# Optimization experiments

Hardware: AMD Instinct MI355X
Metric: run time of the kernel (lower is better)

Reference implementation:

```python
import jax, jax.numpy as jnp
import numpy as np

DIM = 768
NUM_HEADS = 12
HEAD_DIM = DIM // NUM_HEADS
SCALE = HEAD_DIM ** -0.5


def setup_inputs() -> dict:
    key = jax.random.key(0)
    k1, k2, k3, k4 = jax.random.split(key, 4)
    B, H, W = 8, 32, 32
    x = jax.random.normal(k1, (B, H, W, DIM), dtype=jnp.float32)
    s = DIM ** -0.5
    w_qkv = jax.random.normal(k2, (DIM, 3 * DIM), dtype=jnp.float32) * s
    w_proj = jax.random.normal(k3, (DIM, DIM), dtype=jnp.float32) * s
    b_proj = jax.random.normal(k4, (DIM,), dtype=jnp.float32) * 0.01
    return {"x": x, "w_qkv": w_qkv, "w_proj": w_proj, "b_proj": b_proj}


def reference(x, w_qkv, w_proj, b_proj):
    B, H, W, C = x.shape
    N = H * W
    qkv = (x.reshape(B, N, C) @ w_qkv).reshape(B, N, 3, NUM_HEADS, HEAD_DIM)
    q, k, v = jnp.moveaxis(qkv, 2, 0)  # each (B, N, h, d)
    # scores: (B, h, N, N)
    attn = jnp.einsum('bnhd,bmhd->bhnm', q * SCALE, k)
    attn = jax.nn.softmax(attn, axis=-1)
    out = jnp.einsum('bhnm,bmhd->bnhd', attn, v).reshape(B, H, W, C)
    return out @ w_proj + b_proj
```

## Files before the change

kernel.cpp:

```cpp
#include <hip/hip_runtime.h>

typedef _Float16 half_t;
typedef __attribute__((ext_vector_type(4))) _Float16 half4;
typedef __attribute__((ext_vector_type(8))) _Float16 half8;
typedef __attribute__((ext_vector_type(4))) float floatx4;

#define MFMA_F16(A,B,C)  __builtin_amdgcn_mfma_f32_16x16x32_f16(A,B,C,0,0,0)

typedef __attribute__((address_space(1))) const void gvoid_t;
typedef __attribute__((address_space(3))) void svoid_t;

__device__ __forceinline__ void async_copy16(const half_t* g, half_t* l) {
    __builtin_amdgcn_global_load_lds((gvoid_t*)g, (svoid_t*)l, 16, 0, 0);
}

#define QSCALE 0.18033688011112042f

__global__ __launch_bounds__(256)
void prep_kernel(const float* __restrict__ x, const float* __restrict__ w_qkv,
                 const float* __restrict__ w_proj, half_t* __restrict__ xh,
                 half_t* __restrict__ wqkvT, half_t* __restrict__ wprojT)
{
    __shared__ half_t tile[64 * 65];
    const int id = blockIdx.x, tid = threadIdx.x;
    if (id < 6144) {
        size_t e = (size_t)id * 1024 + tid * 4;
        float4 f = *(const float4*)(x + e);
        half4 h = { (half_t)f.x, (half_t)f.y, (half_t)f.z, (half_t)f.w };
        *(half4*)(xh + e) = h;
        return;
    }
    const float* src; half_t* dst; int lds, tr0, tc0;
    if (id < 6576) { int t = id - 6144; src = w_qkv; dst = wqkvT; lds = 2304;
                     tr0 = (t / 36) * 64; tc0 = (t % 36) * 64; }
    else           { int t = id - 6576; src = w_proj; dst = wprojT; lds = 768;
                     tr0 = (t / 12) * 64; tc0 = (t % 12) * 64; }
    #pragma unroll
    for (int i = 0; i < 4; i++) {
        int e = tid + i * 256, r = e >> 4, c4 = (e & 15) << 2;
        float4 f = *(const float4*)(src + (size_t)(tr0 + r) * lds + tc0 + c4);
        tile[(c4 + 0) * 65 + r] = (half_t)f.x;
        tile[(c4 + 1) * 65 + r] = (half_t)f.y;
        tile[(c4 + 2) * 65 + r] = (half_t)f.z;
        tile[(c4 + 3) * 65 + r] = (half_t)f.w;
    }
    __syncthreads();
    #pragma unroll
    for (int i = 0; i < 4; i++) {
        int e = tid + i * 256, c = e >> 4, r4 = (e & 15) << 2;
        half4 h = { tile[c * 65 + r4], tile[c * 65 + r4 + 1],
                    tile[c * 65 + r4 + 2], tile[c * 65 + r4 + 3] };
        *(half4*)(dst + (size_t)(tc0 + c) * 768 + tr0 + r4) = h;
    }
}

__global__ __launch_bounds__(512, 1)
void gemm_qkv(const half_t* __restrict__ A, const half_t* __restrict__ Bt,
              half_t* __restrict__ q_ws, half_t* __restrict__ k_ws,
              half_t* __restrict__ v_ws)
{
    __shared__ half_t As[2][256 * 32];
    __shared__ half_t Bs[2][288 * 32];

    const int lin  = blockIdx.x;
    const int xcd  = lin & 7, rest = lin >> 3;
    const int m0 = ((rest >> 3) * 8 + xcd) * 256;
    const int n0 = (rest & 7) * 288;

    const int tid  = threadIdx.x;
    const int lane = tid & 63;
    const int w    = tid >> 6;
    const int wm   = w >> 1, wn = w & 1;
    const int quad = lane >> 4, l16 = lane & 15;

    const int b0p = (lane ^ (lane >> 2) ^ (lane >> 4)) & 1;
    const int b1p = ((lane >> 1) ^ (lane >> 3)) & 1;
    const int b2p = ((lane >> 2) ^ (lane >> 4)) & 1;
    const int row_log = ((lane >> 2) & 0xC) | ((lane >> 2) & 2) | b2p;
    const int q_log   = (b1p << 1) | b0p;

    const int foff = ((((l16 << 2) | quad) ^ (l16 & 7)) << 3);

    const half_t* aBase = A  + (size_t)(m0 + row_log) * 768 + q_log * 8;
    const half_t* bBase = Bt + (size_t)(n0 + row_log) * 768 + q_log * 8;

    floatx4 acc[4][9];
    #pragma unroll
    for (int i = 0; i < 4; i++)
        #pragma unroll
        for (int j = 0; j < 9; j++) acc[i][j] = (floatx4)0.0f;

    half8 sA0, sA1, sB0, sB1, sB2;

    #define LOADR(KO)                                                          \
        do {                                                                   \
            sA0 = *(const half8*)(aBase + (size_t)((w*2+0)*16) * 768 + (KO));  \
            sA1 = *(const half8*)(aBase + (size_t)((w*2+1)*16) * 768 + (KO));  \
            sB0 = *(const half8*)(bBase + (size_t)((w*2+0)*16) * 768 + (KO));  \
            sB1 = *(const half8*)(bBase + (size_t)((w*2+1)*16) * 768 + (KO));  \
            if (w < 2)                                                         \
                sB2 = *(const half8*)(bBase + (size_t)((16+w)*16) * 768 + (KO)); \
        } while (0)

    #define WRITES(BUF)                                                        \
        do {                                                                   \
            *(half8*)(&As[BUF][(w*2+0)*512 + lane*8]) = sA0;                   \
            *(half8*)(&As[BUF][(w*2+1)*512 + lane*8]) = sA1;                   \
            *(half8*)(&Bs[BUF][(w*2+0)*512 + lane*8]) = sB0;                   \
            *(half8*)(&Bs[BUF][(w*2+1)*512 + lane*8]) = sB1;                   \
            if (w < 2)                                                         \
                *(half8*)(&Bs[BUF][(16+w)*512 + lane*8]) = sB2;                \
        } while (0)

    LOADR(0);
    WRITES(0);
    __syncthreads();

    #pragma unroll 1
    for (int t = 0; t < 24; ++t) {
        const int cur = t & 1;
        if (t < 23) LOADR((t + 1) * 32);

        half8 a[4], b[9];
        #pragma unroll
        for (int mi = 0; mi < 4; mi++)
            a[mi] = *(const half8*)(&As[cur][(wm*4 + mi) * 512 + foff]);
        #pragma unroll
        for (int ni = 0; ni < 9; ni++)
            b[ni] = *(const half8*)(&Bs[cur][(wn*9 + ni) * 512 + foff]);
        __builtin_amdgcn_s_setprio(1);
        #pragma unroll
        for (int mi = 0; mi < 4; mi++)
            #pragma unroll
            for (int ni = 0; ni < 9; ni++)
                acc[mi][ni] = MFMA_F16(a[mi], b[ni], acc[mi][ni]);
        __builtin_amdgcn_s_setprio(0);

        if (t < 23) WRITES(cur ^ 1);
        __syncthreads();
    }
    #undef LOADR
    #undef WRITES

    const int bb  = (m0 + wm * 64) >> 10;
    const int t0w = (m0 + wm * 64) & 1023;

    #pragma unroll
    for (int ni = 0; ni < 9; ni++) {
        const int cb  = n0 + wn * 144 + ni * 16;
        const int sel = (cb >= 1536) ? 2 : (cb >= 768 ? 1 : 0);
        const int rem = cb - sel * 768;
        const int hh  = rem >> 6;
        const int d   = (rem & 63) + l16;
        const size_t base = (size_t)(bb * 12 + hh) * 65536;

        if (sel == 0) {
            #pragma unroll
            for (int mi = 0; mi < 4; mi++) {
                int tok = t0w + mi * 16 + quad * 4;
                half4 hv = { (half_t)(acc[mi][ni][0] * QSCALE),
                             (half_t)(acc[mi][ni][1] * QSCALE),
                             (half_t)(acc[mi][ni][2] * QSCALE),
                             (half_t)(acc[mi][ni][3] * QSCALE) };
                *(half4*)(q_ws + base + (size_t)d * 1024 + tok) = hv;
            }
        } else if (sel == 1) {
            #pragma unroll
            for (int mi = 0; mi < 4; mi++)
                #pragma unroll
                for (int r = 0; r < 4; r++) {
                    int tok = t0w + mi * 16 + quad * 4 + r;
                    k_ws[base + (size_t)tok * 64 + d] = (half_t)acc[mi][ni][r];
                }
        } else {
            #pragma unroll
            for (int mi = 0; mi < 4; mi++) {
                int tokb = t0w + (mi >> 1) * 32;
                int tokp = tokb | (quad << 3) | ((mi & 1) << 2);
                half4 hv = { (half_t)acc[mi][ni][0], (half_t)acc[mi][ni][1],
                             (half_t)acc[mi][ni][2], (half_t)acc[mi][ni][3] };
                *(half4*)(v_ws + base + (size_t)d * 1024 + tokp) = hv;
            }
        }
    }
}

__global__ __launch_bounds__(256, 2)
void gemm_proj(const half_t* __restrict__ A, const half_t* __restrict__ Bt,
               float* __restrict__ Cout, const float* __restrict__ bias)
{
    __shared__ half_t As[2][128 * 32];
    __shared__ half_t Bs[2][192 * 32];

    const int lin  = blockIdx.x;
    const int xcd  = lin & 7, rest = lin >> 3;
    const int m0 = ((rest >> 2) * 8 + xcd) * 128;
    const int n0 = (rest & 3) * 192;

    const int tid  = threadIdx.x;
    const int lane = tid & 63;
    const int w    = tid >> 6;
    const int wm   = w >> 1, wn = w & 1;
    const int quad = lane >> 4, l16 = lane & 15;

    const int b0p = (lane ^ (lane >> 2) ^ (lane >> 4)) & 1;
    const int b1p = ((lane >> 1) ^ (lane >> 3)) & 1;
    const int b2p = ((lane >> 2) ^ (lane >> 4)) & 1;
    const int row_log = ((lane >> 2) & 0xC) | ((lane >> 2) & 2) | b2p;
    const int q_log   = (b1p << 1) | b0p;
    const int foff = ((((l16 << 2) | quad) ^ (l16 & 7)) << 3);

    const half_t* aBase = A  + (size_t)(m0 + row_log) * 768 + q_log * 8;
    const half_t* bBase = Bt + (size_t)(n0 + row_log) * 768 + q_log * 8;

    floatx4 acc[4][6];
    #pragma unroll
    for (int i = 0; i < 4; i++)
        #pragma unroll
        for (int j = 0; j < 6; j++) acc[i][j] = (floatx4)0.0f;

    half8 sA0, sA1, sB0, sB1, sB2;

    #define PLOADR(KO)                                                         \
        do {                                                                   \
            sA0 = *(const half8*)(aBase + (size_t)((w*2+0)*16) * 768 + (KO));  \
            sA1 = *(const half8*)(aBase + (size_t)((w*2+1)*16) * 768 + (KO));  \
            sB0 = *(const half8*)(bBase + (size_t)((w*3+0)*16) * 768 + (KO));  \
            sB1 = *(const half8*)(bBase + (size_t)((w*3+1)*16) * 768 + (KO));  \
            sB2 = *(const half8*)(bBase + (size_t)((w*3+2)*16) * 768 + (KO));  \
        } while (0)

    #define PWRITES(BUF)                                                       \
        do {                                                                   \
            *(half8*)(&As[BUF][(w*2+0)*512 + lane*8]) = sA0;                   \
            *(half8*)(&As[BUF][(w*2+1)*512 + lane*8]) = sA1;                   \
            *(half8*)(&Bs[BUF][(w*3+0)*512 + lane*8]) = sB0;                   \
            *(half8*)(&Bs[BUF][(w*3+1)*512 + lane*8]) = sB1;                   \
            *(half8*)(&Bs[BUF][(w*3+2)*512 + lane*8]) = sB2;                   \
        } while (0)

    PLOADR(0);
    PWRITES(0);
    __syncthreads();

    #pragma unroll 1
    for (int t = 0; t < 24; ++t) {
        const int cur = t & 1;
        if (t < 23) PLOADR((t + 1) * 32);

        half8 a[4], b[6];
        #pragma unroll
        for (int mi = 0; mi < 4; mi++)
            a[mi] = *(const half8*)(&As[cur][(wm*4 + mi) * 512 + foff]);
        #pragma unroll
        for (int ni = 0; ni < 6; ni++)
            b[ni] = *(const half8*)(&Bs[cur][(wn*6 + ni) * 512 + foff]);
        __builtin_amdgcn_s_setprio(1);
        #pragma unroll
        for (int mi = 0; mi < 4; mi++)
            #pragma unroll
            for (int ni = 0; ni < 6; ni++)
                acc[mi][ni] = MFMA_F16(a[mi], b[ni], acc[mi][ni]);
        __builtin_amdgcn_s_setprio(0);

        if (t < 23) PWRITES(cur ^ 1);
        __syncthreads();
    }
    #undef PLOADR
    #undef PWRITES

    float bias_v[6];
    #pragma unroll
    for (int ni = 0; ni < 6; ni++)
        bias_v[ni] = bias[n0 + wn * 96 + ni * 16 + l16];
    float* scratch = (w < 2 ? (float*)As : (float*)Bs) + (w & 1) * 1600;
    #pragma unroll
    for (int mi = 0; mi < 4; mi++) {
        #pragma unroll
        for (int ni = 0; ni < 6; ni++)
            #pragma unroll
            for (int r = 0; r < 4; r++)
                scratch[(quad * 4 + r) * 100 + ni * 16 + l16] =
                    acc[mi][ni][r] + bias_v[ni];
        #pragma unroll
        for (int i = 0; i < 6; i++) {
            int f = quad + i * 4;
            float4 v4 = *(const float4*)(scratch + l16 * 100 + f * 4);
            int gm = m0 + wm * 64 + mi * 16 + l16;
            *(float4*)(Cout + (size_t)gm * 768 + n0 + wn * 96 + f * 4) = v4;
        }
    }
}

__global__ __launch_bounds__(256, 3)
void attn_kernel(const half_t* __restrict__ qT, const half_t* __restrict__ k,
                 const half_t* __restrict__ vT, half_t* __restrict__ a_ws)
{
    __shared__ __align__(16) half_t Kb[2][4096];
    __shared__ __align__(16) half_t Vb[2][4096];
    __shared__ __align__(16) half_t Qs[64 * 128];

    const int lin  = blockIdx.x;
    const int xcd  = lin & 7, rest = lin >> 3;
    const int qc   = rest & 7;
    const int bh   = (rest >> 3) * 8 + xcd;

    const int tid  = threadIdx.x;
    const int lane = tid & 63;
    const int w    = tid >> 6;
    const int quad = lane >> 4, l16 = lane & 15;

    const half_t* qg = qT + (size_t)bh * 65536;
    const half_t* kg = k  + (size_t)bh * 65536;
    const half_t* vg = vT + (size_t)bh * 65536;

    const int srow = lane >> 3;
    const int sch  = (lane & 7) ^ srow;

    #pragma unroll
    for (int j = 0; j < 4; j++) {
        int d0 = w * 16 + j * 4;
        async_copy16(qg + (size_t)(d0 + (lane >> 4)) * 1024 + qc * 128 + (lane & 15) * 8,
                     &Qs[d0 * 128]);
    }
    #pragma unroll
    for (int j = 0; j < 2; j++) {
        int row = j * 32 + w * 8;
        async_copy16(kg + (size_t)(row + srow) * 64 + sch * 8, &Kb[0][row * 64]);
        async_copy16(vg + (size_t)(row + srow) * 1024 + sch * 8, &Vb[0][row * 64]);
    }
    __syncthreads();

    half8 qf[2][2];
    #pragma unroll
    for (int T = 0; T < 2; T++)
        #pragma unroll
        for (int ks = 0; ks < 2; ks++)
            #pragma unroll
            for (int j = 0; j < 8; j++)
                qf[T][ks][j] = Qs[(ks * 32 + quad * 8 + j) * 128
                                  + T * 64 + w * 16 + l16];

    floatx4 acc_o[2][4];
    floatx4 lacc[2];
    #pragma unroll
    for (int T = 0; T < 2; T++) {
        lacc[T] = (floatx4)0.0f;
        #pragma unroll
        for (int dt = 0; dt < 4; dt++) acc_o[T][dt] = (floatx4)0.0f;
    }

    const int xsw = l16 & 7;
    const half8 vone = { (half_t)1.0f, (half_t)1.0f, (half_t)1.0f, (half_t)1.0f,
                         (half_t)1.0f, (half_t)1.0f, (half_t)1.0f, (half_t)1.0f };

    half8 rk0, rk1, rv0, rv1;

    for (int kt = 0; kt < 16; kt++) {
        const int cb = kt & 1;
        __syncthreads();
        if (kt < 15) {
            rk0 = *(const half8*)(kg + (size_t)((kt + 1) * 64 + w * 8 + srow) * 64 + sch * 8);
            rk1 = *(const half8*)(kg + (size_t)((kt + 1) * 64 + 32 + w * 8 + srow) * 64 + sch * 8);
            rv0 = *(const half8*)(vg + (size_t)(w * 8 + srow) * 1024 + (kt + 1) * 64 + sch * 8);
            rv1 = *(const half8*)(vg + (size_t)(32 + w * 8 + srow) * 1024 + (kt + 1) * 64 + sch * 8);
        }
        const half_t* Kc = Kb[cb];
        const half_t* Vc = Vb[cb];

        floatx4 sc[2][4];
        #pragma unroll
        for (int T = 0; T < 2; T++)
            #pragma unroll
            for (int mt = 0; mt < 4; mt++) sc[T][mt] = (floatx4)0.0f;
        __builtin_amdgcn_s_setprio(1);
        #pragma unroll
        for (int ks = 0; ks < 2; ks++)
            #pragma unroll
            for (int mt = 0; mt < 4; mt++) {
                half8 kf = *(const half8*)(Kc + (mt * 16 + l16) * 64
                                              + (((ks << 2) + quad) ^ xsw) * 8);
                sc[0][mt] = MFMA_F16(kf, qf[0][ks], sc[0][mt]);
                sc[1][mt] = MFMA_F16(kf, qf[1][ks], sc[1][mt]);
            }
        __builtin_amdgcn_s_setprio(0);

        half8 pa[2][2];
        #pragma unroll
        for (int T = 0; T < 2; T++)
            #pragma unroll
            for (int g = 0; g < 2; g++) {
                half8 ph;
                #pragma unroll
                for (int r = 0; r < 4; r++) ph[r]     = (half_t)exp2f(sc[T][2 * g][r]);
                #pragma unroll
                for (int r = 0; r < 4; r++) ph[4 + r] = (half_t)exp2f(sc[T][2 * g + 1][r]);
                pa[T][g] = ph;
            }

        __builtin_amdgcn_s_setprio(1);
        #pragma unroll
        for (int g = 0; g < 2; g++) {
            lacc[0] = MFMA_F16(pa[0][g], vone, lacc[0]);
            lacc[1] = MFMA_F16(pa[1][g], vone, lacc[1]);
            #pragma unroll
            for (int dt = 0; dt < 4; dt++) {
                half8 vb = *(const half8*)(Vc + (dt * 16 + l16) * 64
                                              + ((((g << 2) + quad) ^ xsw) << 3));
                acc_o[0][dt] = MFMA_F16(pa[0][g], vb, acc_o[0][dt]);
                acc_o[1][dt] = MFMA_F16(pa[1][g], vb, acc_o[1][dt]);
            }
        }
        __builtin_amdgcn_s_setprio(0);

        if (kt < 15) {
            *(half8*)(&Kb[cb ^ 1][(w * 8) * 64 + lane * 8])      = rk0;
            *(half8*)(&Kb[cb ^ 1][(32 + w * 8) * 64 + lane * 8]) = rk1;
            *(half8*)(&Vb[cb ^ 1][(w * 8) * 64 + lane * 8])      = rv0;
            *(half8*)(&Vb[cb ^ 1][(32 + w * 8) * 64 + lane * 8]) = rv1;
        }
    }

    const int b = bh / 12, h = bh - (bh / 12) * 12;
    #pragma unroll
    for (int T = 0; T < 2; T++)
        #pragma unroll
        for (int r = 0; r < 4; r++) {
            float inv = 1.0f / lacc[T][r];
            int n = qc * 128 + T * 64 + w * 16 + quad * 4 + r;
            half_t* op = a_ws + ((size_t)(b * 1024 + n)) * 768 + h * 64;
            #pragma unroll
            for (int dt = 0; dt < 4; dt++)
                op[dt * 16 + l16] = (half_t)(acc_o[T][dt][r] * inv);
        }
}

extern "C" void kernel_launch(void* const* d_in, const int* in_sizes, int n_in,
                              void* d_out, int out_size, void* d_ws, size_t ws_size,
                              hipStream_t stream)
{
    (void)in_sizes; (void)n_in; (void)out_size; (void)ws_size;
    const float* x      = (const float*)d_in[0];
    const float* w_qkv  = (const float*)d_in[1];
    const float* w_proj = (const float*)d_in[2];
    const float* b_proj = (const float*)d_in[3];
    float* out = (float*)d_out;

    half_t* ws     = (half_t*)d_ws;
    half_t* q_ws   = ws;
    half_t* k_ws   = ws + 6291456;
    half_t* v_ws   = ws + 2 * 6291456;
    half_t* xh     = ws + 3 * 6291456;
    half_t* wqkvT  = ws + 4 * 6291456;
    half_t* wprojT = wqkvT + 1769472;
    half_t* a_ws   = xh;

    prep_kernel<<<dim3(6720), dim3(256), 0, stream>>>(x, w_qkv, w_proj, xh, wqkvT, wprojT);
    gemm_qkv<<<dim3(256), dim3(512), 0, stream>>>(xh, wqkvT, q_ws, k_ws, v_ws);
    attn_kernel<<<dim3(768), dim3(256), 0, stream>>>(q_ws, k_ws, v_ws, a_ws);
    gemm_proj<<<dim3(256), dim3(256), 0, stream>>>(a_ws, wprojT, out, b_proj);
}
```

Baseline: 184.8 us.

## Fuse x fp32-to-fp16 conversion into QKV GEMM loads and drop setprio hints

```diff
diff --git a/kernel.cpp b/kernel.cpp
--- a/kernel.cpp
+++ b/kernel.cpp
@@ -17,24 +17,16 @@
 #define QSCALE 0.18033688011112042f
 
 __global__ __launch_bounds__(256)
-void prep_kernel(const float* __restrict__ x, const float* __restrict__ w_qkv,
-                 const float* __restrict__ w_proj, half_t* __restrict__ xh,
+void prep_kernel(const float* __restrict__ w_qkv, const float* __restrict__ w_proj,
                  half_t* __restrict__ wqkvT, half_t* __restrict__ wprojT)
 {
     __shared__ half_t tile[64 * 65];
     const int id = blockIdx.x, tid = threadIdx.x;
-    if (id < 6144) {
-        size_t e = (size_t)id * 1024 + tid * 4;
-        float4 f = *(const float4*)(x + e);
-        half4 h = { (half_t)f.x, (half_t)f.y, (half_t)f.z, (half_t)f.w };
-        *(half4*)(xh + e) = h;
-        return;
-    }
     const float* src; half_t* dst; int lds, tr0, tc0;
-    if (id < 6576) { int t = id - 6144; src = w_qkv; dst = wqkvT; lds = 2304;
-                     tr0 = (t / 36) * 64; tc0 = (t % 36) * 64; }
-    else           { int t = id - 6576; src = w_proj; dst = wprojT; lds = 768;
-                     tr0 = (t / 12) * 64; tc0 = (t % 12) * 64; }
+    if (id < 432) { src = w_qkv; dst = wqkvT; lds = 2304;
+                    tr0 = (id / 36) * 64; tc0 = (id % 36) * 64; }
+    else          { int t = id - 432; src = w_proj; dst = wprojT; lds = 768;
+                    tr0 = (t / 12) * 64; tc0 = (t % 12) * 64; }
     #pragma unroll
     for (int i = 0; i < 4; i++) {
         int e = tid + i * 256, r = e >> 4, c4 = (e & 15) << 2;
@@ -55,7 +47,7 @@
 }
 
 __global__ __launch_bounds__(512, 1)
-void gemm_qkv(const half_t* __restrict__ A, const half_t* __restrict__ Bt,
+void gemm_qkv(const float* __restrict__ X, const half_t* __restrict__ Bt,
               half_t* __restrict__ q_ws, half_t* __restrict__ k_ws,
               half_t* __restrict__ v_ws)
 {
@@ -81,7 +73,7 @@
 
     const int foff = ((((l16 << 2) | quad) ^ (l16 & 7)) << 3);
 
-    const half_t* aBase = A  + (size_t)(m0 + row_log) * 768 + q_log * 8;
+    const float*  aBase = X  + (size_t)(m0 + row_log) * 768 + q_log * 8;
     const half_t* bBase = Bt + (size_t)(n0 + row_log) * 768 + q_log * 8;
 
     floatx4 acc[4][9];
@@ -90,12 +82,15 @@
         #pragma unroll
         for (int j = 0; j < 9; j++) acc[i][j] = (floatx4)0.0f;
 
-    half8 sA0, sA1, sB0, sB1, sB2;
+    float4 fa00, fa01, fa10, fa11;
+    half8 sB0, sB1, sB2;
 
     #define LOADR(KO)                                                          \
         do {                                                                   \
-            sA0 = *(const half8*)(aBase + (size_t)((w*2+0)*16) * 768 + (KO));  \
-            sA1 = *(const half8*)(aBase + (size_t)((w*2+1)*16) * 768 + (KO));  \
+            fa00 = *(const float4*)(aBase + (size_t)((w*2+0)*16) * 768 + (KO));      \
+            fa01 = *(const float4*)(aBase + (size_t)((w*2+0)*16) * 768 + (KO) + 4);  \
+            fa10 = *(const float4*)(aBase + (size_t)((w*2+1)*16) * 768 + (KO));      \
+            fa11 = *(const float4*)(aBase + (size_t)((w*2+1)*16) * 768 + (KO) + 4);  \
             sB0 = *(const half8*)(bBase + (size_t)((w*2+0)*16) * 768 + (KO));  \
             sB1 = *(const half8*)(bBase + (size_t)((w*2+1)*16) * 768 + (KO));  \
             if (w < 2)                                                         \
@@ -104,8 +99,14 @@
 
     #define WRITES(BUF)                                                        \
         do {                                                                   \
-            *(half8*)(&As[BUF][(w*2+0)*512 + lane*8]) = sA0;                   \
-            *(half8*)(&As[BUF][(w*2+1)*512 + lane*8]) = sA1;                   \
+            half8 h0 = { (half_t)fa00.x, (half_t)fa00.y, (half_t)fa00.z,       \
+                         (half_t)fa00.w, (half_t)fa01.x, (half_t)fa01.y,       \
+                         (half_t)fa01.z, (half_t)fa01.w };                     \
+            half8 h1 = { (half_t)fa10.x, (half_t)fa10.y, (half_t)fa10.z,       \
+                         (half_t)fa10.w, (half_t)fa11.x, (half_t)fa11.y,       \
+                         (half_t)fa11.z, (half_t)fa11.w };                     \
+            *(half8*)(&As[BUF][(w*2+0)*512 + lane*8]) = h0;                    \
+            *(half8*)(&As[BUF][(w*2+1)*512 + lane*8]) = h1;                    \
             *(half8*)(&Bs[BUF][(w*2+0)*512 + lane*8]) = sB0;                   \
             *(half8*)(&Bs[BUF][(w*2+1)*512 + lane*8]) = sB1;                   \
             if (w < 2)                                                         \
@@ -128,13 +129,11 @@
         #pragma unroll
         for (int ni = 0; ni < 9; ni++)
             b[ni] = *(const half8*)(&Bs[cur][(wn*9 + ni) * 512 + foff]);
-        __builtin_amdgcn_s_setprio(1);
         #pragma unroll
         for (int mi = 0; mi < 4; mi++)
             #pragma unroll
             for (int ni = 0; ni < 9; ni++)
                 acc[mi][ni] = MFMA_F16(a[mi], b[ni], acc[mi][ni]);
-        __builtin_amdgcn_s_setprio(0);
 
         if (t < 23) WRITES(cur ^ 1);
         __syncthreads();
@@ -255,13 +254,11 @@
         #pragma unroll
         for (int ni = 0; ni < 6; ni++)
             b[ni] = *(const half8*)(&Bs[cur][(wn*6 + ni) * 512 + foff]);
-        __builtin_amdgcn_s_setprio(1);
         #pragma unroll
         for (int mi = 0; mi < 4; mi++)
             #pragma unroll
             for (int ni = 0; ni < 6; ni++)
                 acc[mi][ni] = MFMA_F16(a[mi], b[ni], acc[mi][ni]);
-        __builtin_amdgcn_s_setprio(0);
 
         if (t < 23) PWRITES(cur ^ 1);
         __syncthreads();
@@ -373,7 +370,6 @@
         for (int T = 0; T < 2; T++)
             #pragma unroll
             for (int mt = 0; mt < 4; mt++) sc[T][mt] = (floatx4)0.0f;
-        __builtin_amdgcn_s_setprio(1);
         #pragma unroll
         for (int ks = 0; ks < 2; ks++)
             #pragma unroll
@@ -383,7 +379,6 @@
                 sc[0][mt] = MFMA_F16(kf, qf[0][ks], sc[0][mt]);
                 sc[1][mt] = MFMA_F16(kf, qf[1][ks], sc[1][mt]);
             }
-        __builtin_amdgcn_s_setprio(0);
 
         half8 pa[2][2];
         #pragma unroll
@@ -398,7 +393,6 @@
                 pa[T][g] = ph;
             }
 
-        __builtin_amdgcn_s_setprio(1);
         #pragma unroll
         for (int g = 0; g < 2; g++) {
             lacc[0] = MFMA_F16(pa[0][g], vone, lacc[0]);
@@ -411,7 +405,6 @@
                 acc_o[1][dt] = MFMA_F16(pa[1][g], vb, acc_o[1][dt]);
             }
         }
-        __builtin_amdgcn_s_setprio(0);
 
         if (kt < 15) {
             *(half8*)(&Kb[cb ^ 1][(w * 8) * 64 + lane * 8])      = rk0;
@@ -450,13 +443,12 @@
     half_t* q_ws   = ws;
     half_t* k_ws   = ws + 6291456;
     half_t* v_ws   = ws + 2 * 6291456;
-    half_t* xh     = ws + 3 * 6291456;
+    half_t* a_ws   = ws + 3 * 6291456;
     half_t* wqkvT  = ws + 4 * 6291456;
     half_t* wprojT = wqkvT + 1769472;
-    half_t* a_ws   = xh;
-
-    prep_kernel<<<dim3(6720), dim3(256), 0, stream>>>(x, w_qkv, w_proj, xh, wqkvT, wprojT);
-    gemm_qkv<<<dim3(256), dim3(512), 0, stream>>>(xh, wqkvT, q_ws, k_ws, v_ws);
+
+    prep_kernel<<<dim3(576), dim3(256), 0, stream>>>(w_qkv, w_proj, wqkvT, wprojT);
+    gemm_qkv<<<dim3(256), dim3(512), 0, stream>>>(x, wqkvT, q_ws, k_ws, v_ws);
     attn_kernel<<<dim3(768), dim3(256), 0, stream>>>(q_ws, k_ws, v_ws, a_ws);
     gemm_proj<<<dim3(256), dim3(256), 0, stream>>>(a_ws, wprojT, out, b_proj);
 }
```

New measurement: 191.2 us. 1.03x slower.
